# Kernel tuning notes

Measured on AMD Instinct MI355X. Metric: run time of the kernel, lower is better.

The kernel has to match this reference:

```python
import jax, jax.numpy as jnp
import numpy as np

EPS = 1e-6
B, CLASSES, DISTR, C, H, W = 32, 16, 8, 64, 16, 16


def setup_inputs() -> dict:
    key = jax.random.key(0)
    ks = jax.random.split(key, 6)
    x_LE = jax.random.uniform(ks[0], (B, 4, C, H, W), dtype=jnp.float32)
    labels = jax.random.randint(ks[1], (B,), 0, CLASSES)
    X_LEs = jnp.zeros((CLASSES, 2, C, H, W), jnp.float32) + EPS
    X_LEs_xy = jnp.zeros((CLASSES, 2, C, H, W), jnp.float32) + EPS
    X_weights = jnp.zeros((CLASSES, 1), jnp.float32) + EPS
    sigmas = jnp.ones((CLASSES,), jnp.float32)
    w1 = jax.random.uniform(ks[2], (DISTR,), dtype=jnp.float32)
    miu = jax.random.uniform(ks[3], (DISTR, 2, C, H, W), dtype=jnp.float32)
    tao = jax.random.uniform(ks[4], (DISTR,), dtype=jnp.float32)
    weight = jax.random.uniform(ks[5], (3,), dtype=jnp.float32)
    return dict(x_LE=x_LE, labels=labels, X_LEs=X_LEs, X_LEs_xy=X_LEs_xy,
                X_weights=X_weights, sigmas=sigmas, w1=w1, miu=miu, tao=tao,
                weight=weight)


def reference(x_LE, labels, X_LEs, X_LEs_xy, X_weights, sigmas, w1, miu, tao, weight):
    ls = jax.nn.log_sigmoid
    Bn = x_LE.shape[0]
    classes, num_distr = X_LEs.shape[0], tao.shape[0]
    in_ch, Hh, Ww = x_LE.shape[2], x_LE.shape[3], x_LE.shape[4]

    x_tm = x_LE[:, :2]   # theta/mag  [B,2,C,H,W]
    x_xy = x_LE[:, 2:]   # xy         [B,2,C,H,W]

    # source normalizes w1 for BOTH w1 and w2 (faithful to original bug)
    w1n = w1 ** 2 / jnp.sum(w1 ** 2)
    w2n = w1n

    # label-indexed scatter_add into persistent class buffers (detached)
    seg = lambda v: jax.ops.segment_sum(v.reshape(Bn, -1), labels, num_segments=classes)
    X_LEs_u = jax.lax.stop_gradient(X_LEs + seg(x_tm).reshape(X_LEs.shape))
    X_LEs_xy_u = jax.lax.stop_gradient(X_LEs_xy + seg(x_xy).reshape(X_LEs_xy.shape))
    counts = jax.ops.segment_sum(jnp.ones((Bn, 1), x_LE.dtype), labels, num_segments=classes)
    X_w = jax.lax.stop_gradient(X_weights + counts)  # [K,1]

    xle_out = (X_LEs_u.reshape(classes, -1) / X_w).reshape(X_LEs.shape)  # [K,2,C,H,W]

    sigma_sq = sigmas ** 2  # [K]
    tao_sq = tao ** 2       # [D]

    # ---- SURE loss (labels branch) ----
    t_dc = tao_sq[:, None]                                 # [D,K]
    term1 = sigma_sq / (t_dc + sigma_sq) ** 2              # [D,K]
    le_miu = (ls(xle_out[:, None]) - ls(miu[None])) ** 2   # [K,D,2,C,H,W]
    le_norm = jnp.sum(le_miu.reshape(classes, num_distr, -1), axis=2).T  # [D,K]
    term2 = sigma_sq[None, :] * le_norm
    term3 = 2.0 * in_ch * Hh * Ww * (t_dc ** 2 - sigma_sq[None, :] ** 2) / X_w[:, 0][None, :]
    loss = jnp.mean(term1 * (term2 + term3), axis=1)       # [D]

    # ---- class means (James-Stein shrinkage) ----
    t_cd = tao_sq[None, :]                                 # [K,D]
    s_cd = sigma_sq[:, None]                               # [K,D]
    a = (t_cd / (s_cd + t_cd))[:, :, None, None, None]     # [K,D,1,1,1]
    b = (s_cd / (s_cd + t_cd))[:, :, None, None, None]
    mag = xle_out[:, None, 1]                              # [K,1,C,H,W]
    wb = w1n[None, :, None, None, None]
    means_mag = jnp.sum(jnp.exp((a * ls(mag + EPS) + b * ls(miu[None, :, 1] + EPS)) * wb), axis=1)  # [K,C,H,W]
    # NOTE: source uses mag channel for the theta mean too (faithful)
    means_theta = jnp.sum((mag * a + miu[None, :, 0] * b) * w2n[None, :, None, None, None], axis=1)  # [K,C,H,W]

    # ---- distances, broadcast over (classes, batch) ----
    dist_rot = jnp.abs(x_tm[None, :, 0] - means_theta[:, None])                 # [K,B,C,H,W]
    dist_abs = jnp.abs(jnp.log(x_tm[None, :, 1] / (means_mag[:, None] + EPS)))  # [K,B,C,H,W]
    xy_out = (X_LEs_xy_u.reshape(classes, -1) / X_w).reshape(X_LEs_xy.shape)    # [K,2,C,H,W]
    dist_xy = jnp.sum((x_xy[None] - xy_out[:, None]) ** 2, axis=2)              # [K,B,C,H,W]

    dist = weight[0] ** 2 * dist_rot + weight[1] ** 2 * dist_abs + weight[2] ** 2 * dist_xy
    # permute+MaxPool1d(kernel=classes) of -dist, negated back == min over classes
    out = jnp.min(dist, axis=0)  # [B,C,H,W]
    return out, loss
```

## Files before the change

kernel.cpp:

```cpp
#include <hip/hip_runtime.h>
#include <math.h>

#define EPSF 1e-6f
constexpr int Bn  = 32;
constexpr int CLS = 16;
constexpr int DST = 8;
constexpr int Cc  = 64, Hh = 16, Wd = 16;
constexpr int CHW  = Cc * Hh * Wd;
constexpr int CHW2 = 2 * CHW;
constexpr int CHW4 = 4 * CHW;
constexpr int KCHUNK = 64;

__device__ __forceinline__ float fls(float x) {
    float t = __expf(-fabsf(x));
    return fminf(x, 0.0f) - __logf(1.0f + t);
}

__device__ __forceinline__ float4 ld4(const float* p) { return *(const float4*)p; }
__device__ __forceinline__ void st4(float* p, float4 v) { *(float4*)p = v; }

__global__ __launch_bounds__(256) void k1(
                   const float* __restrict__ x, const int* __restrict__ labels,
                   const float* __restrict__ X_LEs, const float* __restrict__ X_LEs_xy,
                   const float* __restrict__ X_weights, const float* __restrict__ miu,
                   float* __restrict__ xle_out, float* __restrict__ xy_out,
                   float* __restrict__ lm0a, float* __restrict__ lm1a,
                   float* __restrict__ lm1ea)
{
    if (blockIdx.x >= 512) {
        const int idx = (blockIdx.x - 512) * 256 + threadIdx.x;
        const int d  = idx >> 12;
        const int e4 = (idx & 4095) << 2;
        const float4 m0 = ld4(miu + d * CHW2 + e4);
        const float4 m1 = ld4(miu + d * CHW2 + CHW + e4);
        float4 r0, r1, r1e;
        r0.x = fls(m0.x); r0.y = fls(m0.y); r0.z = fls(m0.z); r0.w = fls(m0.w);
        r1.x = fls(m1.x); r1.y = fls(m1.y); r1.z = fls(m1.z); r1.w = fls(m1.w);
        r1e.x = fls(m1.x + EPSF); r1e.y = fls(m1.y + EPSF);
        r1e.z = fls(m1.z + EPSF); r1e.w = fls(m1.w + EPSF);
        st4(lm0a  + d * CHW + e4, r0);
        st4(lm1a  + d * CHW + e4, r1);
        st4(lm1ea + d * CHW + e4, r1e);
        return;
    }

    const int c  = blockIdx.x >> 5;
    const int t  = (blockIdx.x & 31) * 256 + threadIdx.x;
    const int e4 = t << 2;

    __shared__ int lab_sh[Bn];
    if (threadIdx.x < Bn) lab_sh[threadIdx.x] = labels[threadIdx.x];
    __syncthreads();

    float4 acc_tm = {0.f,0.f,0.f,0.f}, acc_xy = {0.f,0.f,0.f,0.f};
    float cnt = 0.f;
    for (int b = 0; b < Bn; ++b) {
        if (lab_sh[b] == c) {
            const float4 xt = ld4(x + b * CHW4 + e4);
            const float4 xx = ld4(x + b * CHW4 + CHW2 + e4);
            acc_tm.x += xt.x; acc_tm.y += xt.y; acc_tm.z += xt.z; acc_tm.w += xt.w;
            acc_xy.x += xx.x; acc_xy.y += xx.y; acc_xy.z += xx.z; acc_xy.w += xx.w;
            cnt += 1.0f;
        }
    }

    const float xw = X_weights[c] + cnt;
    const float4 le  = ld4(X_LEs    + c * CHW2 + e4);
    const float4 xy  = ld4(X_LEs_xy + c * CHW2 + e4);
    float4 o1, o2;
    o1.x = (le.x + acc_tm.x) / xw; o1.y = (le.y + acc_tm.y) / xw;
    o1.z = (le.z + acc_tm.z) / xw; o1.w = (le.w + acc_tm.w) / xw;
    o2.x = (xy.x + acc_xy.x) / xw; o2.y = (xy.y + acc_xy.y) / xw;
    o2.z = (xy.z + acc_xy.z) / xw; o2.w = (xy.w + acc_xy.w) / xw;
    st4(xle_out + c * CHW2 + e4, o1);
    st4(xy_out  + c * CHW2 + e4, o2);
}

__global__ __launch_bounds__(256) void k2(
                   const float* __restrict__ xle_out, const float* __restrict__ miu,
                   const float* __restrict__ sigmas, const float* __restrict__ tao,
                   const float* __restrict__ w1,
                   const float* __restrict__ lm0a, const float* __restrict__ lm1a,
                   const float* __restrict__ lm1ea,
                   float* __restrict__ means_theta, float* __restrict__ lmm_out,
                   float* __restrict__ partials)
{
    const int c     = blockIdx.x >> 6;
    const int chunk = blockIdx.x & 63;
    const int e     = chunk * blockDim.x + threadIdx.x;

    const float sig    = sigmas[c];
    const float sig_sq = sig * sig;

    float w1sqv[DST];
    float ssum = 0.f;
#pragma unroll
    for (int d = 0; d < DST; ++d) { const float t = w1[d]; w1sqv[d] = t * t; ssum += t * t; }
    const float ssum_r = 1.0f / ssum;

    const float xle0 = xle_out[c * CHW2 + e];
    const float xle1 = xle_out[c * CHW2 + CHW + e];
    const float ls0  = fls(xle0);
    const float ls1  = fls(xle1);
    const float ls1e = fls(xle1 + EPSF);

    float mt = 0.f, mm = 0.f;
    float ln_d[DST];

#pragma unroll
    for (int d = 0; d < DST; ++d) {
        const float ta     = tao[d];
        const float tao_sq = ta * ta;
        const float den_r  = 1.0f / (sig_sq + tao_sq);
        const float a      = tao_sq * den_r;
        const float b      = sig_sq * den_r;
        const float wn     = w1sqv[d] * ssum_r;

        const float m0   = miu[d * CHW2 + e];
        const float lm0  = lm0a [d * CHW + e];
        const float lm1  = lm1a [d * CHW + e];
        const float lm1e = lm1ea[d * CHW + e];

        mt += (xle1 * a + m0 * b) * wn;
        mm += __expf((a * ls1e + b * lm1e) * wn);

        const float d0 = ls0 - lm0, d1 = ls1 - lm1;
        ln_d[d] = d0 * d0 + d1 * d1;
    }

    means_theta[c * CHW + e] = mt;
    lmm_out    [c * CHW + e] = __logf(mm + EPSF);

    __shared__ float sh[4][DST];
    const int wave = threadIdx.x >> 6;
    const int lane = threadIdx.x & 63;
#pragma unroll
    for (int d = 0; d < DST; ++d) {
        float v = ln_d[d];
        v += __shfl_down(v, 32);
        v += __shfl_down(v, 16);
        v += __shfl_down(v, 8);
        v += __shfl_down(v, 4);
        v += __shfl_down(v, 2);
        v += __shfl_down(v, 1);
        if (lane == 0) sh[wave][d] = v;
    }
    __syncthreads();
    if (threadIdx.x < DST) {
        const int d = threadIdx.x;
        const float s = sh[0][d] + sh[1][d] + sh[2][d] + sh[3][d];
        partials[(d * CLS + c) * KCHUNK + chunk] = s;
    }
}

__global__ __launch_bounds__(256) void k3(
                   const float* __restrict__ x, const float* __restrict__ weight,
                   const float* __restrict__ means_theta, const float* __restrict__ lmm,
                   const float* __restrict__ xy_out,
                   const int* __restrict__ labels, const float* __restrict__ X_weights,
                   const float* __restrict__ sigmas, const float* __restrict__ tao,
                   const float* __restrict__ partials,
                   float* __restrict__ out, float* __restrict__ loss_out)
{
    if (blockIdx.x == 512) {
        const int t = threadIdx.x;
        if (t >= 128) return;
        const int d = t >> 4;
        const int c = t & 15;

        const float* p = partials + (d * CLS + c) * KCHUNK;
        float le = 0.f;
#pragma unroll
        for (int k = 0; k < KCHUNK; ++k) le += p[k];

        float cnt = 0.f;
        for (int b = 0; b < Bn; ++b) cnt += (labels[b] == c) ? 1.f : 0.f;
        const float xw = X_weights[c] + cnt;

        const float sig = sigmas[c], ssq = sig * sig;
        const float ta  = tao[d],    tsq = ta * ta;
        const float den = tsq + ssq;

        const float term1 = ssq / (den * den);
        const float term2 = ssq * le;
        const float term3 = (2.0f * (float)CHW) * (tsq * tsq - ssq * ssq) / xw;

        float v = term1 * (term2 + term3);
        v += __shfl_xor(v, 8);
        v += __shfl_xor(v, 4);
        v += __shfl_xor(v, 2);
        v += __shfl_xor(v, 1);
        if (c == 0) loss_out[d] = v * (1.0f / 16.0f);
        return;
    }

    const int idx = blockIdx.x * 256 + threadIdx.x;
    const int b  = idx >> 12;
    const int e4 = (idx & 4095) << 2;

    const float w0 = weight[0], w1w = weight[1], w2 = weight[2];
    const float w0sq = w0 * w0, w1sq = w1w * w1w, w2sq = w2 * w2;

    const float* xb = x + b * CHW4;
    const float4 xt0 = ld4(xb + e4);
    const float4 xt1 = ld4(xb + CHW + e4);
    const float4 xx0 = ld4(xb + CHW2 + e4);
    const float4 xx1 = ld4(xb + CHW2 + CHW + e4);
    float4 lx;
    lx.x = __logf(xt1.x); lx.y = __logf(xt1.y);
    lx.z = __logf(xt1.z); lx.w = __logf(xt1.w);

    float4 m = { __builtin_inff(), __builtin_inff(), __builtin_inff(), __builtin_inff() };
#pragma unroll
    for (int c = 0; c < CLS; ++c) {
        const float4 mtv = ld4(means_theta + c * CHW + e4);
        const float4 lmv = ld4(lmm + c * CHW + e4);
        const float4 y0  = ld4(xy_out + c * CHW2 + e4);
        const float4 y1  = ld4(xy_out + c * CHW2 + CHW + e4);

        {
            const float dr = fabsf(xt0.x - mtv.x);
            const float da = fabsf(lx.x - lmv.x);
            const float d0 = xx0.x - y0.x, d1 = xx1.x - y1.x;
            m.x = fminf(m.x, w0sq * dr + w1sq * da + w2sq * (d0 * d0 + d1 * d1));
        }
        {
            const float dr = fabsf(xt0.y - mtv.y);
            const float da = fabsf(lx.y - lmv.y);
            const float d0 = xx0.y - y0.y, d1 = xx1.y - y1.y;
            m.y = fminf(m.y, w0sq * dr + w1sq * da + w2sq * (d0 * d0 + d1 * d1));
        }
        {
            const float dr = fabsf(xt0.z - mtv.z);
            const float da = fabsf(lx.z - lmv.z);
            const float d0 = xx0.z - y0.z, d1 = xx1.z - y1.z;
            m.z = fminf(m.z, w0sq * dr + w1sq * da + w2sq * (d0 * d0 + d1 * d1));
        }
        {
            const float dr = fabsf(xt0.w - mtv.w);
            const float da = fabsf(lx.w - lmv.w);
            const float d0 = xx0.w - y0.w, d1 = xx1.w - y1.w;
            m.w = fminf(m.w, w0sq * dr + w1sq * da + w2sq * (d0 * d0 + d1 * d1));
        }
    }
    st4(out + b * CHW + e4, m);
}

extern "C" void kernel_launch(void* const* d_in, const int* in_sizes, int n_in,
                              void* d_out, int out_size, void* d_ws, size_t ws_size,
                              hipStream_t stream)
{
    const float* x         = (const float*)d_in[0];
    const int*   labels    = (const int*)  d_in[1];
    const float* X_LEs     = (const float*)d_in[2];
    const float* X_LEs_xy  = (const float*)d_in[3];
    const float* X_weights = (const float*)d_in[4];
    const float* sigmas    = (const float*)d_in[5];
    const float* w1        = (const float*)d_in[6];
    const float* miu       = (const float*)d_in[7];
    const float* tao       = (const float*)d_in[8];
    const float* weight    = (const float*)d_in[9];

    float* ws          = (float*)d_ws;
    float* xle_out     = ws;
    float* xy_out      = ws + 524288;
    float* means_theta = ws + 1048576;
    float* lmm         = ws + 1310720;
    float* partials    = ws + 1572864;
    float* lm0a        = ws + 1581056;
    float* lm1a        = ws + 1712128;
    float* lm1ea       = ws + 1843200;

    float* out  = (float*)d_out;
    float* loss = out + Bn * CHW;

    hipLaunchKernelGGL(k1, dim3(512 + 128), dim3(256), 0, stream,
                       x, labels, X_LEs, X_LEs_xy, X_weights, miu,
                       xle_out, xy_out, lm0a, lm1a, lm1ea);
    hipLaunchKernelGGL(k2, dim3(CLS * KCHUNK), dim3(256), 0, stream,
                       xle_out, miu, sigmas, tao, w1, lm0a, lm1a, lm1ea,
                       means_theta, lmm, partials);
    hipLaunchKernelGGL(k3, dim3(512 + 1), dim3(256), 0, stream,
                       x, weight, means_theta, lmm, xy_out,
                       labels, X_weights, sigmas, tao, partials,
                       out, loss);
}
```

Baseline: 95.81 us.

## Fuse class-accumulation and mean/SURE kernels, recompute miu log-sigmoids inline

Merges the first two kernels into one, so each thread accumulates the label-matched batch sums and computes the class means and SURE partial sums directly. This removes the xle_out round trip and one kernel launch. The precomputed log-sigmoid tables for miu are dropped and recomputed per class in the inner loop, which trades extra transcendental work (16x redundant across classes) for fewer memory passes. Loads also go from float4 to scalar in the accumulation.

```diff
diff --git a/kernel.cpp b/kernel.cpp
--- a/kernel.cpp
+++ b/kernel.cpp
@@ -19,75 +19,40 @@
 __device__ __forceinline__ float4 ld4(const float* p) { return *(const float4*)p; }
 __device__ __forceinline__ void st4(float* p, float4 v) { *(float4*)p = v; }
 
-__global__ __launch_bounds__(256) void k1(
-                   const float* __restrict__ x, const int* __restrict__ labels,
-                   const float* __restrict__ X_LEs, const float* __restrict__ X_LEs_xy,
-                   const float* __restrict__ X_weights, const float* __restrict__ miu,
-                   float* __restrict__ xle_out, float* __restrict__ xy_out,
-                   float* __restrict__ lm0a, float* __restrict__ lm1a,
-                   float* __restrict__ lm1ea)
+__global__ __launch_bounds__(256) void K1(
+    const float* __restrict__ x, const int* __restrict__ labels,
+    const float* __restrict__ X_LEs, const float* __restrict__ X_LEs_xy,
+    const float* __restrict__ X_weights, const float* __restrict__ sigmas,
+    const float* __restrict__ w1, const float* __restrict__ miu,
+    const float* __restrict__ tao,
+    float* __restrict__ xy_out, float* __restrict__ means_theta,
+    float* __restrict__ lmm, float* __restrict__ partials)
 {
-    if (blockIdx.x >= 512) {
-        const int idx = (blockIdx.x - 512) * 256 + threadIdx.x;
-        const int d  = idx >> 12;
-        const int e4 = (idx & 4095) << 2;
-        const float4 m0 = ld4(miu + d * CHW2 + e4);
-        const float4 m1 = ld4(miu + d * CHW2 + CHW + e4);
-        float4 r0, r1, r1e;
-        r0.x = fls(m0.x); r0.y = fls(m0.y); r0.z = fls(m0.z); r0.w = fls(m0.w);
-        r1.x = fls(m1.x); r1.y = fls(m1.y); r1.z = fls(m1.z); r1.w = fls(m1.w);
-        r1e.x = fls(m1.x + EPSF); r1e.y = fls(m1.y + EPSF);
-        r1e.z = fls(m1.z + EPSF); r1e.w = fls(m1.w + EPSF);
-        st4(lm0a  + d * CHW + e4, r0);
-        st4(lm1a  + d * CHW + e4, r1);
-        st4(lm1ea + d * CHW + e4, r1e);
-        return;
-    }
-
-    const int c  = blockIdx.x >> 5;
-    const int t  = (blockIdx.x & 31) * 256 + threadIdx.x;
-    const int e4 = t << 2;
+    const int c     = blockIdx.x >> 6;
+    const int chunk = blockIdx.x & 63;
+    const int e     = chunk * 256 + threadIdx.x;
 
     __shared__ int lab_sh[Bn];
     if (threadIdx.x < Bn) lab_sh[threadIdx.x] = labels[threadIdx.x];
     __syncthreads();
 
-    float4 acc_tm = {0.f,0.f,0.f,0.f}, acc_xy = {0.f,0.f,0.f,0.f};
-    float cnt = 0.f;
+    float acc_tm0 = 0.f, acc_tm1 = 0.f, acc_xy0 = 0.f, acc_xy1 = 0.f, cnt = 0.f;
     for (int b = 0; b < Bn; ++b) {
         if (lab_sh[b] == c) {
-            const float4 xt = ld4(x + b * CHW4 + e4);
-            const float4 xx = ld4(x + b * CHW4 + CHW2 + e4);
-            acc_tm.x += xt.x; acc_tm.y += xt.y; acc_tm.z += xt.z; acc_tm.w += xt.w;
-            acc_xy.x += xx.x; acc_xy.y += xx.y; acc_xy.z += xx.z; acc_xy.w += xx.w;
+            const float* xb = x + b * CHW4;
+            acc_tm0 += xb[e];
+            acc_tm1 += xb[CHW + e];
+            acc_xy0 += xb[CHW2 + e];
+            acc_xy1 += xb[CHW2 + CHW + e];
             cnt += 1.0f;
         }
     }
-
     const float xw = X_weights[c] + cnt;
-    const float4 le  = ld4(X_LEs    + c * CHW2 + e4);
-    const float4 xy  = ld4(X_LEs_xy + c * CHW2 + e4);
-    float4 o1, o2;
-    o1.x = (le.x + acc_tm.x) / xw; o1.y = (le.y + acc_tm.y) / xw;
-    o1.z = (le.z + acc_tm.z) / xw; o1.w = (le.w + acc_tm.w) / xw;
-    o2.x = (xy.x + acc_xy.x) / xw; o2.y = (xy.y + acc_xy.y) / xw;
-    o2.z = (xy.z + acc_xy.z) / xw; o2.w = (xy.w + acc_xy.w) / xw;
-    st4(xle_out + c * CHW2 + e4, o1);
-    st4(xy_out  + c * CHW2 + e4, o2);
-}
-
-__global__ __launch_bounds__(256) void k2(
-                   const float* __restrict__ xle_out, const float* __restrict__ miu,
-                   const float* __restrict__ sigmas, const float* __restrict__ tao,
-                   const float* __restrict__ w1,
-                   const float* __restrict__ lm0a, const float* __restrict__ lm1a,
-                   const float* __restrict__ lm1ea,
-                   float* __restrict__ means_theta, float* __restrict__ lmm_out,
-                   float* __restrict__ partials)
-{
-    const int c     = blockIdx.x >> 6;
-    const int chunk = blockIdx.x & 63;
-    const int e     = chunk * blockDim.x + threadIdx.x;
+
+    const float xle0 = (X_LEs[c * CHW2 + e]       + acc_tm0) / xw;
+    const float xle1 = (X_LEs[c * CHW2 + CHW + e] + acc_tm1) / xw;
+    xy_out[c * CHW2 + e]       = (X_LEs_xy[c * CHW2 + e]       + acc_xy0) / xw;
+    xy_out[c * CHW2 + CHW + e] = (X_LEs_xy[c * CHW2 + CHW + e] + acc_xy1) / xw;
 
     const float sig    = sigmas[c];
     const float sig_sq = sig * sig;
@@ -98,8 +63,6 @@
     for (int d = 0; d < DST; ++d) { const float t = w1[d]; w1sqv[d] = t * t; ssum += t * t; }
     const float ssum_r = 1.0f / ssum;
 
-    const float xle0 = xle_out[c * CHW2 + e];
-    const float xle1 = xle_out[c * CHW2 + CHW + e];
     const float ls0  = fls(xle0);
     const float ls1  = fls(xle1);
     const float ls1e = fls(xle1 + EPSF);
@@ -117,9 +80,10 @@
         const float wn     = w1sqv[d] * ssum_r;
 
         const float m0   = miu[d * CHW2 + e];
-        const float lm0  = lm0a [d * CHW + e];
-        const float lm1  = lm1a [d * CHW + e];
-        const float lm1e = lm1ea[d * CHW + e];
+        const float m1   = miu[d * CHW2 + CHW + e];
+        const float lm0  = fls(m0);
+        const float lm1  = fls(m1);
+        const float lm1e = fls(m1 + EPSF);
 
         mt += (xle1 * a + m0 * b) * wn;
         mm += __expf((a * ls1e + b * lm1e) * wn);
@@ -129,7 +93,7 @@
     }
 
     means_theta[c * CHW + e] = mt;
-    lmm_out    [c * CHW + e] = __logf(mm + EPSF);
+    lmm        [c * CHW + e] = __logf(mm + EPSF);
 
     __shared__ float sh[4][DST];
     const int wave = threadIdx.x >> 6;
@@ -153,14 +117,14 @@
     }
 }
 
-__global__ __launch_bounds__(256) void k3(
-                   const float* __restrict__ x, const float* __restrict__ weight,
-                   const float* __restrict__ means_theta, const float* __restrict__ lmm,
-                   const float* __restrict__ xy_out,
-                   const int* __restrict__ labels, const float* __restrict__ X_weights,
-                   const float* __restrict__ sigmas, const float* __restrict__ tao,
-                   const float* __restrict__ partials,
-                   float* __restrict__ out, float* __restrict__ loss_out)
+__global__ __launch_bounds__(256) void K2(
+    const float* __restrict__ x, const float* __restrict__ weight,
+    const float* __restrict__ means_theta, const float* __restrict__ lmm,
+    const float* __restrict__ xy_out,
+    const int* __restrict__ labels, const float* __restrict__ X_weights,
+    const float* __restrict__ sigmas, const float* __restrict__ tao,
+    const float* __restrict__ partials,
+    float* __restrict__ out, float* __restrict__ loss_out)
 {
     if (blockIdx.x == 512) {
         const int t = threadIdx.x;
@@ -217,7 +181,6 @@
         const float4 lmv = ld4(lmm + c * CHW + e4);
         const float4 y0  = ld4(xy_out + c * CHW2 + e4);
         const float4 y1  = ld4(xy_out + c * CHW2 + CHW + e4);
-
         {
             const float dr = fabsf(xt0.x - mtv.x);
             const float da = fabsf(lx.x - lmv.x);
@@ -262,25 +225,19 @@
     const float* weight    = (const float*)d_in[9];
 
     float* ws          = (float*)d_ws;
-    float* xle_out     = ws;
-    float* xy_out      = ws + 524288;
-    float* means_theta = ws + 1048576;
-    float* lmm         = ws + 1310720;
-    float* partials    = ws + 1572864;
-    float* lm0a        = ws + 1581056;
-    float* lm1a        = ws + 1712128;
-    float* lm1ea       = ws + 1843200;
+    float* xy_out      = ws;
+    float* means_theta = ws + 524288;
+    float* lmm         = ws + 786432;
+    float* partials    = ws + 1048576;
 
     float* out  = (float*)d_out;
     float* loss = out + Bn * CHW;
 
-    hipLaunchKernelGGL(k1, dim3(512 + 128), dim3(256), 0, stream,
-                       x, labels, X_LEs, X_LEs_xy, X_weights, miu,
-                       xle_out, xy_out, lm0a, lm1a, lm1ea);
-    hipLaunchKernelGGL(k2, dim3(CLS * KCHUNK), dim3(256), 0, stream,
-                       xle_out, miu, sigmas, tao, w1, lm0a, lm1a, lm1ea,
-                       means_theta, lmm, partials);
-    hipLaunchKernelGGL(k3, dim3(512 + 1), dim3(256), 0, stream,
+    hipLaunchKernelGGL(K1, dim3(CLS * KCHUNK), dim3(256), 0, stream,
+                       x, labels, X_LEs, X_LEs_xy, X_weights, sigmas,
+                       w1, miu, tao,
+                       xy_out, means_theta, lmm, partials);
+    hipLaunchKernelGGL(K2, dim3(512 + 1), dim3(256), 0, stream,
                        x, weight, means_theta, lmm, xy_out,
                        labels, X_weights, sigmas, tao, partials,
                        out, loss);
```

New measurement: 97.17 us. Within noise of the previous version (+1.4%).
